# Kernel optimization log

Measured on AMD Instinct MI355X. Metric: run time of the kernel, lower is better.

Reference implementation:

```python
import jax, jax.numpy as jnp
import numpy as np

N = 20000      # nodes
E = 320000     # edges (before self-loops)
F_IN = 512     # input feature size
HID = 128      # encoder hidden
OUT = 128      # encoder output / GAT in_channels
H = 4          # gat heads
C = 64         # gat out_channels per head


def setup_inputs() -> dict:
    key = jax.random.key(0)
    ks = jax.random.split(key, 10)
    s = 0.05
    return {
        "x": jax.random.normal(ks[0], (N, F_IN), jnp.float32),
        "edge_index": jax.random.randint(ks[1], (2, E), 0, N, dtype=jnp.int64),
        "W1": jax.random.normal(ks[2], (F_IN, HID), jnp.float32) * s,
        "b1": jax.random.normal(ks[3], (HID,), jnp.float32) * s,
        "W2": jax.random.normal(ks[4], (HID, OUT), jnp.float32) * s,
        "b2": jax.random.normal(ks[5], (OUT,), jnp.float32) * s,
        "Wg": jax.random.normal(ks[6], (OUT, H * C), jnp.float32) * s,
        "att_src": jax.random.normal(ks[7], (H, C), jnp.float32) * s,
        "att_dst": jax.random.normal(ks[8], (H, C), jnp.float32) * s,
        "bias_g": jax.random.normal(ks[9], (H * C,), jnp.float32) * s,
    }


def reference(x, edge_index, W1, b1, W2, b2, Wg, att_src, att_dst, bias_g):
    # MLP encoder: Linear -> ReLU -> Linear
    h = jnp.maximum(x @ W1 + b1, 0.0) @ W2 + b2            # [N, OUT]

    # GATConv (concat=True, eval mode -> no dropout)
    xg = (h @ Wg).reshape(N, H, C)                          # per-head projections

    # add self-loops (PyG GATConv default)
    loops = jnp.arange(N, dtype=edge_index.dtype)
    src = jnp.concatenate([edge_index[0], loops])           # [E+N] source j
    dst = jnp.concatenate([edge_index[1], loops])           # [E+N] dest   i

    a_src = jnp.einsum('nhc,hc->nh', xg, att_src)           # [N, H]
    a_dst = jnp.einsum('nhc,hc->nh', xg, att_dst)           # [N, H]

    e = jax.nn.leaky_relu(a_src[src] + a_dst[dst], 0.2)     # [E+N, H]

    # segment softmax over incoming edges of each destination node
    m = jax.ops.segment_max(e, dst, num_segments=N)         # [N, H]
    ex = jnp.exp(e - m[dst])
    denom = jax.ops.segment_sum(ex, dst, num_segments=N)
    alpha = ex / (denom[dst] + 1e-16)                       # [E+N, H]

    # weighted scatter-add aggregation
    out = jax.ops.segment_sum(alpha[:, :, None] * xg[src], dst, num_segments=N)  # [N, H, C]
    return out.reshape(N, H * C) + bias_g
```

## Files before the change

### kernel.cpp

```cpp
#include <hip/hip_runtime.h>
#include <math.h>

#define NNODES 20000
#define NEDGES 320000
#define FIN    512
#define HIDD   128
#define OUTD   128
#define NH     4
#define NC     64
#define HC     256

typedef short bf16x8 __attribute__((ext_vector_type(8)));
typedef float f32x4  __attribute__((ext_vector_type(4)));

__device__ __forceinline__ unsigned short f2bf(float f) {
    unsigned int u = __float_as_uint(f);
    unsigned int r = 0x7fffu + ((u >> 16) & 1u);
    return (unsigned short)((u + r) >> 16);
}
__device__ __forceinline__ float b2f(short t) {
    return __uint_as_float(((unsigned)(unsigned short)t) << 16);
}

#define PREP_TB1 64
#define PREP_TB2 192
__global__ __launch_bounds__(256)
void prep_kernel(const float* __restrict__ W1, unsigned short* __restrict__ W1t,
                 const float* __restrict__ W2, const float* __restrict__ b2,
                 const float* __restrict__ Wg, unsigned short* __restrict__ W2gt,
                 float* __restrict__ b2g, int* __restrict__ deg, int n) {
    const int bid = blockIdx.x;
    const int tid = threadIdx.x;
    if (bid < PREP_TB1) {
        __shared__ float tile[32][33];
        const int tk = bid >> 2;
        const int tn = bid & 3;
        const int k0 = tk * 32, n0 = tn * 32;
        const int nin = tid & 31;
        const int r8  = tid >> 5;
        #pragma unroll
        for (int s = 0; s < 4; ++s) {
            int k = s * 8 + r8;
            tile[k][nin] = W1[(size_t)(k0 + k) * HIDD + n0 + nin];
        }
        __syncthreads();
        #pragma unroll
        for (int s = 0; s < 4; ++s) {
            int nn = s * 8 + r8;
            W1t[(size_t)(n0 + nn) * FIN + k0 + nin] = f2bf(tile[nin][nn]);
        }
    } else if (bid < PREP_TB2) {
        int local = (bid - PREP_TB1) * 256 + tid;
        int nn = local >> 7;
        int k  = local & 127;
        float s = 0.f;
        #pragma unroll 8
        for (int t = 0; t < HIDD; ++t)
            s += W2[(size_t)k * OUTD + t] * Wg[(size_t)t * HC + nn];
        W2gt[(size_t)nn * HIDD + k] = f2bf(s);
        if (k == 0) {
            float t2 = 0.f;
            #pragma unroll 8
            for (int t = 0; t < OUTD; ++t) t2 += b2[t] * Wg[(size_t)t * HC + nn];
            b2g[nn] = t2;
        }
    } else {
        int i = (bid - PREP_TB2) * 256 + tid;
        if (i < n) deg[i] = 1;
    }
}

__global__ __launch_bounds__(256)
void gemm1_count_kernel(const float* __restrict__ A,
                        const unsigned short* __restrict__ Bt,
                        const float* __restrict__ bias,
                        unsigned short* __restrict__ C,
                        const int* __restrict__ dst, int* __restrict__ deg,
                        int M, int E, int gemmBlocks) {
    __shared__ unsigned short As[32 * 64];
    __shared__ unsigned short Bs[128 * 64];

    if ((int)blockIdx.x >= gemmBlocks) {
        int base = ((int)blockIdx.x - gemmBlocks) * 1024 + threadIdx.x;
        #pragma unroll
        for (int t = 0; t < 4; ++t) {
            int i = base + t * 256;
            if (i < E) atomicAdd(&deg[dst[i]], 1);
        }
        return;
    }

    const int tid  = threadIdx.x;
    const int lane = tid & 63;
    const int w    = tid >> 6;
    const int wr   = w >> 1;
    const int wc   = w & 1;
    const int m0   = blockIdx.x * 32;

    char* pA = (char*)As;
    char* pB = (char*)Bs;

    f32x4 acc[4];
    #pragma unroll
    for (int n = 0; n < 4; ++n) acc[n] = (f32x4){0.f, 0.f, 0.f, 0.f};

    for (int k0 = 0; k0 < FIN; k0 += 64) {
        {
            const int row = tid >> 3;
            const int sg  = tid & 7;
            const bool ok = (m0 + row) < M;
            const float4* Ap = (const float4*)(A + (size_t)(m0 + row) * FIN + k0 + sg * 8);
            float4 f0 = make_float4(0,0,0,0), f1 = f0;
            if (ok) { f0 = Ap[0]; f1 = Ap[1]; }
            unsigned short u[8];
            u[0]=f2bf(f0.x); u[1]=f2bf(f0.y); u[2]=f2bf(f0.z); u[3]=f2bf(f0.w);
            u[4]=f2bf(f1.x); u[5]=f2bf(f1.y); u[6]=f2bf(f1.z); u[7]=f2bf(f1.w);
            *(bf16x8*)(pA + (((row * 128 + sg * 16)) ^ ((row & 7) << 4))) = *(bf16x8*)&u[0];
        }
        #pragma unroll
        for (int i = 0; i < 4; ++i) {
            int s   = tid + i * 256;
            int col = s >> 3;
            int sg  = s & 7;
            bf16x8 v = *(const bf16x8*)(Bt + (size_t)col * FIN + k0 + sg * 8);
            *(bf16x8*)(pB + (((col * 128 + sg * 16)) ^ ((col & 7) << 4))) = v;
        }
        __syncthreads();

        #pragma unroll
        for (int ks = 0; ks < 2; ++ks) {
            const int kb = ks * 64 + ((lane >> 4) << 4);
            int row = wr * 16 + (lane & 15);
            bf16x8 a = *(const bf16x8*)(pA + ((row * 128 + kb) ^ ((row & 7) << 4)));
            bf16x8 b[4];
            #pragma unroll
            for (int n = 0; n < 4; ++n) {
                int col = wc * 64 + n * 16 + (lane & 15);
                b[n] = *(const bf16x8*)(pB + ((col * 128 + kb) ^ ((col & 7) << 4)));
            }
            #pragma unroll
            for (int n = 0; n < 4; ++n)
                acc[n] = __builtin_amdgcn_mfma_f32_16x16x32_bf16(a, b[n], acc[n], 0, 0, 0);
        }
        __syncthreads();
    }

    #pragma unroll
    for (int n = 0; n < 4; ++n) {
        const int col = wc * 64 + n * 16 + (lane & 15);
        const float bv = bias[col];
        #pragma unroll
        for (int r = 0; r < 4; ++r) {
            const int row = m0 + wr * 16 + ((lane >> 4) << 2) + r;
            if (row >= M) continue;
            float v = fmaxf(acc[n][r] + bv, 0.f);
            C[(size_t)row * HIDD + col] = f2bf(v);
        }
    }
}

__global__ __launch_bounds__(1024)
void scan_offsets_kernel(const int* __restrict__ deg, int* __restrict__ offs,
                         int* __restrict__ cursor, int* __restrict__ csr, int n) {
    __shared__ int wsum[16], wbase[16];
    const int tid = threadIdx.x, lane = tid & 63, w = tid >> 6;
    const int i0 = tid * 20;
    int loc[20];
    int s = 0;
    #pragma unroll
    for (int k = 0; k < 20; ++k) {
        int i = i0 + k;
        int v = (i < n) ? deg[i] : 0;
        loc[k] = s;
        s += v;
    }
    int incl = s;
    #pragma unroll
    for (int d = 1; d < 64; d <<= 1) {
        int t = __shfl_up(incl, d);
        if (lane >= d) incl += t;
    }
    if (lane == 63) wsum[w] = incl;
    __syncthreads();
    if (w == 0) {
        int v = (lane < 16) ? wsum[lane] : 0;
        int sc = v;
        #pragma unroll
        for (int d = 1; d < 16; d <<= 1) {
            int t = __shfl_up(sc, d);
            if (lane >= d) sc += t;
        }
        if (lane < 16) wbase[lane] = sc - v;
    }
    __syncthreads();
    const int excl = wbase[w] + incl - s;
    #pragma unroll
    for (int k = 0; k < 20; ++k) {
        int i = i0 + k;
        if (i < n) {
            int o = excl + loc[k];
            offs[i]   = o;
            cursor[i] = o + 1;
            csr[o]    = i;
        }
    }
    if (tid == 1023) offs[n] = excl + s;
}

__global__ __launch_bounds__(256)
void gemm2_dots_scatter_kernel(const unsigned short* __restrict__ Ab,
                               const unsigned short* __restrict__ Bt,
                               const float* __restrict__ b2g,
                               const float* __restrict__ att_src,
                               const float* __restrict__ att_dst,
                               unsigned short* __restrict__ xgh,
                               float* __restrict__ a_src, float* __restrict__ a_dst,
                               const int* __restrict__ e_src, const int* __restrict__ e_dst,
                               int* __restrict__ cursor, int* __restrict__ csr,
                               int M, int E, int gemmBlocks) {
    const int tid = threadIdx.x;

    if ((int)blockIdx.x >= gemmBlocks) {
        int i = ((int)blockIdx.x - gemmBlocks) * 256 + tid;
        if (i < E) {
            int s = e_src[i], d = e_dst[i];
            csr[atomicAdd(&cursor[d], 1)] = s;
        }
        return;
    }

    __shared__ unsigned short As[64 * 64];
    __shared__ unsigned short Bs[128 * 64];

    const int lane = tid & 63;
    const int w    = tid >> 6;
    const int wr   = w >> 1;
    const int wc   = w & 1;
    const int m0   = ((int)blockIdx.x >> 1) * 64;
    const int n0   = ((int)blockIdx.x & 1) * 128;

    char* pA = (char*)As;
    char* pB = (char*)Bs;

    f32x4 acc[2][4];
    #pragma unroll
    for (int m = 0; m < 2; ++m)
        #pragma unroll
        for (int n = 0; n < 4; ++n) acc[m][n] = (f32x4){0.f, 0.f, 0.f, 0.f};

    for (int k0 = 0; k0 < HIDD; k0 += 64) {
        #pragma unroll
        for (int i = 0; i < 2; ++i) {
            int s   = tid + i * 256;
            int row = s >> 3;
            int sg  = s & 7;
            bf16x8 v = {};
            if ((m0 + row) < M)
                v = *(const bf16x8*)(Ab + (size_t)(m0 + row) * HIDD + k0 + sg * 8);
            *(bf16x8*)(pA + (((row * 128 + sg * 16)) ^ ((row & 7) << 4))) = v;
        }
        #pragma unroll
        for (int i = 0; i < 4; ++i) {
            int s   = tid + i * 256;
            int col = s >> 3;
            int sg  = s & 7;
            bf16x8 v = *(const bf16x8*)(Bt + (size_t)(n0 + col) * HIDD + k0 + sg * 8);
            *(bf16x8*)(pB + (((col * 128 + sg * 16)) ^ ((col & 7) << 4))) = v;
        }
        __syncthreads();

        #pragma unroll
        for (int ks = 0; ks < 2; ++ks) {
            const int kb = ks * 64 + ((lane >> 4) << 4);
            bf16x8 a[2], b[4];
            #pragma unroll
            for (int m = 0; m < 2; ++m) {
                int row = wr * 32 + m * 16 + (lane & 15);
                a[m] = *(const bf16x8*)(pA + ((row * 128 + kb) ^ ((row & 7) << 4)));
            }
            #pragma unroll
            for (int n = 0; n < 4; ++n) {
                int col = wc * 64 + n * 16 + (lane & 15);
                b[n] = *(const bf16x8*)(pB + ((col * 128 + kb) ^ ((col & 7) << 4)));
            }
            #pragma unroll
            for (int m = 0; m < 2; ++m)
                #pragma unroll
                for (int n = 0; n < 4; ++n)
                    acc[m][n] = __builtin_amdgcn_mfma_f32_16x16x32_bf16(
                        a[m], b[n], acc[m][n], 0, 0, 0);
        }
        __syncthreads();
    }

    const int head = ((int)blockIdx.x & 1) * 2 + wc;
    const int cIn  = lane & 15;
    unsigned short* plane = xgh + (size_t)head * M * NC;
    float ds_p[2][4], dd_p[2][4];
    #pragma unroll
    for (int m = 0; m < 2; ++m)
        #pragma unroll
        for (int r = 0; r < 4; ++r) { ds_p[m][r] = 0.f; dd_p[m][r] = 0.f; }

    #pragma unroll
    for (int n = 0; n < 4; ++n) {
        const int ch  = n * 16 + cIn;
        const int col = n0 + wc * 64 + n * 16 + cIn;
        const float bv   = b2g[col];
        const float as_c = att_src[head * NC + ch];
        const float ad_c = att_dst[head * NC + ch];
        #pragma unroll
        for (int m = 0; m < 2; ++m) {
            #pragma unroll
            for (int r = 0; r < 4; ++r) {
                const int row = m0 + wr * 32 + m * 16 + ((lane >> 4) << 2) + r;
                float v = acc[m][n][r] + bv;
                if (row < M) plane[(size_t)row * NC + ch] = f2bf(v);
                ds_p[m][r] += v * as_c;
                dd_p[m][r] += v * ad_c;
            }
        }
    }
    #pragma unroll
    for (int m = 0; m < 2; ++m) {
        #pragma unroll
        for (int r = 0; r < 4; ++r) {
            float s = ds_p[m][r], d = dd_p[m][r];
            s += __shfl_xor(s, 1); s += __shfl_xor(s, 2);
            s += __shfl_xor(s, 4); s += __shfl_xor(s, 8);
            d += __shfl_xor(d, 1); d += __shfl_xor(d, 2);
            d += __shfl_xor(d, 4); d += __shfl_xor(d, 8);
            if (cIn == 0) {
                const int row = m0 + wr * 32 + m * 16 + ((lane >> 4) << 2) + r;
                if (row < M) {
                    a_src[row * NH + head] = s;
                    a_dst[row * NH + head] = d;
                }
            }
        }
    }
}

__global__ __launch_bounds__(256)
void gat_aggregate6_kernel(const unsigned short* __restrict__ xgh,
                           const float* __restrict__ asrc,
                           const float* __restrict__ adst,
                           const int* __restrict__ offs, const int* __restrict__ csr,
                           const float* __restrict__ bias, float* __restrict__ out,
                           int n, int nbPerHead) {
    const int wv   = threadIdx.x >> 6;
    const int lane = threadIdx.x & 63;
    const int head = (int)blockIdx.x / nbPerHead;
    const int node = ((int)blockIdx.x % nbPerHead) * 4 + wv;
    if (node >= n) return;
    const int g = lane >> 3;
    const int q = lane & 7;
    const int beg = offs[node];
    const int deg = offs[node + 1] - beg;
    const float adh = adst[node * NH + head];
    const unsigned short* plane = xgh + (size_t)head * n * NC;

    float acc[8] = {0.f, 0.f, 0.f, 0.f, 0.f, 0.f, 0.f, 0.f};
    float den = 0.f;

    for (int c0 = 0; c0 < deg; c0 += 64) {
        const int j = c0 + lane;
        int   s_l = 0;
        float w_l = 0.f;
        if (j < deg) {
            s_l = csr[beg + j];
            float e = asrc[s_l * NH + head] + adh;
            e = e > 0.f ? e : 0.2f * e;
            w_l = __expf(e);
        }
        den += w_l;

        const int cn = (deg - c0 < 64) ? (deg - c0) : 64;
        #pragma unroll
        for (int t = 0; t < 8; ++t) {
            if (t * 8 >= cn) break;
            const int jj = t * 8 + g;
            const float wgt = __shfl(w_l, jj);
            const int   s   = __shfl(s_l, jj);
            if (jj < cn) {
                bf16x8 v = *(const bf16x8*)(plane + (size_t)s * NC + q * 8);
                #pragma unroll
                for (int u = 0; u < 8; ++u) acc[u] += wgt * b2f(v[u]);
            }
        }
    }

    #pragma unroll
    for (int mask = 1; mask <= 32; mask <<= 1) den += __shfl_xor(den, mask);
    #pragma unroll
    for (int mask = 8; mask <= 32; mask <<= 1) {
        #pragma unroll
        for (int t = 0; t < 8; ++t) acc[t] += __shfl_xor(acc[t], mask);
    }

    if (g == 0) {
        const float inv = 1.f / (den + 1e-16f);
        const int cb = head * NC + q * 8;
        const int base = node * HC + cb;
        float4 o0 = make_float4(acc[0] * inv + bias[cb + 0],
                                acc[1] * inv + bias[cb + 1],
                                acc[2] * inv + bias[cb + 2],
                                acc[3] * inv + bias[cb + 3]);
        float4 o1 = make_float4(acc[4] * inv + bias[cb + 4],
                                acc[5] * inv + bias[cb + 5],
                                acc[6] * inv + bias[cb + 6],
                                acc[7] * inv + bias[cb + 7]);
        *(float4*)(out + base)     = o0;
        *(float4*)(out + base + 4) = o1;
    }
}

extern "C" void kernel_launch(void* const* d_in, const int* in_sizes, int n_in,
                              void* d_out, int out_size, void* d_ws, size_t ws_size,
                              hipStream_t stream) {
    const float* x       = (const float*)d_in[0];
    const int*   ei      = (const int*)d_in[1];
    const float* W1      = (const float*)d_in[2];
    const float* b1      = (const float*)d_in[3];
    const float* W2      = (const float*)d_in[4];
    const float* b2      = (const float*)d_in[5];
    const float* Wg      = (const float*)d_in[6];
    const float* att_src = (const float*)d_in[7];
    const float* att_dst = (const float*)d_in[8];
    const float* bias_g  = (const float*)d_in[9];

    const int Nn = in_sizes[0] / FIN;
    const int E  = in_sizes[1] / 2;
    const int* e_src = ei;
    const int* e_dst = ei + E;

    char* w = (char*)d_ws;
    auto alloc = [&](size_t bytes) { char* p = w; w += (bytes + 255) & ~(size_t)255; return p; };
    unsigned short* W1t  = (unsigned short*)alloc((size_t)OUTD * FIN * 2);
    unsigned short* W2gt = (unsigned short*)alloc((size_t)HC * HIDD * 2);
    float* b2g  = (float*)alloc(HC * 4);
    unsigned short* h1  = (unsigned short*)alloc((size_t)Nn * HIDD * 2);
    unsigned short* xgh = (unsigned short*)alloc((size_t)NH * Nn * NC * 2);
    float* asrc = (float*)alloc((size_t)Nn * NH * 4);
    float* adst = (float*)alloc((size_t)Nn * NH * 4);
    int* deg    = (int*)alloc((size_t)Nn * 4);
    int* offs   = (int*)alloc((size_t)(Nn + 1) * 4);
    int* cursor = (int*)alloc((size_t)Nn * 4);
    int* csr    = (int*)alloc((size_t)(E + Nn) * 4);

    dim3 blk(256);

    {
        int nb = PREP_TB2 + (Nn + 255) / 256;
        prep_kernel<<<dim3(nb), blk, 0, stream>>>(
            W1, W1t, W2, b2, Wg, W2gt, b2g, deg, Nn);
    }

    {
        int gb = (Nn + 31) / 32;
        int cb = (E + 1023) / 1024;
        gemm1_count_kernel<<<dim3(gb + cb), blk, 0, stream>>>(
            x, W1t, b1, h1, e_dst, deg, Nn, E, gb);
    }

    scan_offsets_kernel<<<dim3(1), dim3(1024), 0, stream>>>(deg, offs, cursor, csr, Nn);

    {
        int gb = ((Nn + 63) / 64) * 2;
        int sb = (E + 255) / 256;
        gemm2_dots_scatter_kernel<<<dim3(gb + sb), blk, 0, stream>>>(
            h1, W2gt, b2g, att_src, att_dst, xgh, asrc, adst,
            e_src, e_dst, cursor, csr, Nn, E, gb);
    }

    {
        int nbPerHead = (Nn + 3) / 4;
        gat_aggregate6_kernel<<<dim3(NH * nbPerHead), blk, 0, stream>>>(
            xgh, asrc, adst, offs, csr, bias_g, (float*)d_out, Nn, nbPerHead);
    }
}
```

Before: 137.4 us.

## Use 16-bit CSR indices, head-major attention scores, move degree counting to prep

Stores CSR source indices as 16-bit values, which relies on the node count fitting in 16 bits. Switches a_src/a_dst to a head-major layout so each aggregate wave gathers from a contiguous per-head array. Degree counting moves from the gemm1 launch into the prep kernel, with a memset replacing the init-to-one and the +1 for self-loops added in the scan. Bf16 unpacking also switches to uint4 lo/hi bit tricks. The aim is to cut gather bandwidth in aggregation, at the cost of an extra memset launch and an index width that limits the node count.

Measured after the change: 141.8 us. +3.3%, slower.

```diff
diff --git a/kernel.cpp b/kernel.cpp
--- a/kernel.cpp
+++ b/kernel.cpp
@@ -18,17 +18,21 @@
     unsigned int r = 0x7fffu + ((u >> 16) & 1u);
     return (unsigned short)((u + r) >> 16);
 }
-__device__ __forceinline__ float b2f(short t) {
-    return __uint_as_float(((unsigned)(unsigned short)t) << 16);
+__device__ __forceinline__ float bflo(unsigned int u) {
+    return __uint_as_float(u << 16);
+}
+__device__ __forceinline__ float bfhi(unsigned int u) {
+    return __uint_as_float(u & 0xffff0000u);
 }
 
 #define PREP_TB1 64
 #define PREP_TB2 192
 __global__ __launch_bounds__(256)
-void prep_kernel(const float* __restrict__ W1, unsigned short* __restrict__ W1t,
-                 const float* __restrict__ W2, const float* __restrict__ b2,
-                 const float* __restrict__ Wg, unsigned short* __restrict__ W2gt,
-                 float* __restrict__ b2g, int* __restrict__ deg, int n) {
+void prep_count_kernel(const float* __restrict__ W1, unsigned short* __restrict__ W1t,
+                       const float* __restrict__ W2, const float* __restrict__ b2,
+                       const float* __restrict__ Wg, unsigned short* __restrict__ W2gt,
+                       float* __restrict__ b2g,
+                       const int* __restrict__ e_dst, int* __restrict__ deg, int E) {
     const int bid = blockIdx.x;
     const int tid = threadIdx.x;
     if (bid < PREP_TB1) {
@@ -66,29 +70,17 @@
         }
     } else {
         int i = (bid - PREP_TB2) * 256 + tid;
-        if (i < n) deg[i] = 1;
+        if (i < E) atomicAdd(&deg[e_dst[i]], 1);
     }
 }
 
 __global__ __launch_bounds__(256)
-void gemm1_count_kernel(const float* __restrict__ A,
-                        const unsigned short* __restrict__ Bt,
-                        const float* __restrict__ bias,
-                        unsigned short* __restrict__ C,
-                        const int* __restrict__ dst, int* __restrict__ deg,
-                        int M, int E, int gemmBlocks) {
+void gemm1_kernel(const float* __restrict__ A,
+                  const unsigned short* __restrict__ Bt,
+                  const float* __restrict__ bias,
+                  unsigned short* __restrict__ C, int M) {
     __shared__ unsigned short As[32 * 64];
     __shared__ unsigned short Bs[128 * 64];
-
-    if ((int)blockIdx.x >= gemmBlocks) {
-        int base = ((int)blockIdx.x - gemmBlocks) * 1024 + threadIdx.x;
-        #pragma unroll
-        for (int t = 0; t < 4; ++t) {
-            int i = base + t * 256;
-            if (i < E) atomicAdd(&deg[dst[i]], 1);
-        }
-        return;
-    }
 
     const int tid  = threadIdx.x;
     const int lane = tid & 63;
@@ -161,7 +153,8 @@
 
 __global__ __launch_bounds__(1024)
 void scan_offsets_kernel(const int* __restrict__ deg, int* __restrict__ offs,
-                         int* __restrict__ cursor, int* __restrict__ csr, int n) {
+                         int* __restrict__ cursor, unsigned short* __restrict__ csr16,
+                         int n) {
     __shared__ int wsum[16], wbase[16];
     const int tid = threadIdx.x, lane = tid & 63, w = tid >> 6;
     const int i0 = tid * 20;
@@ -170,7 +163,7 @@
     #pragma unroll
     for (int k = 0; k < 20; ++k) {
         int i = i0 + k;
-        int v = (i < n) ? deg[i] : 0;
+        int v = (i < n) ? (deg[i] + 1) : 0;
         loc[k] = s;
         s += v;
     }
@@ -199,9 +192,9 @@
         int i = i0 + k;
         if (i < n) {
             int o = excl + loc[k];
-            offs[i]   = o;
-            cursor[i] = o + 1;
-            csr[o]    = i;
+            offs[i]    = o;
+            cursor[i]  = o + 1;
+            csr16[o]   = (unsigned short)i;
         }
     }
     if (tid == 1023) offs[n] = excl + s;
@@ -214,9 +207,10 @@
                                const float* __restrict__ att_src,
                                const float* __restrict__ att_dst,
                                unsigned short* __restrict__ xgh,
-                               float* __restrict__ a_src, float* __restrict__ a_dst,
+                               float* __restrict__ a_src,
+                               float* __restrict__ a_dst,
                                const int* __restrict__ e_src, const int* __restrict__ e_dst,
-                               int* __restrict__ cursor, int* __restrict__ csr,
+                               int* __restrict__ cursor, unsigned short* __restrict__ csr16,
                                int M, int E, int gemmBlocks) {
     const int tid = threadIdx.x;
 
@@ -224,7 +218,7 @@
         int i = ((int)blockIdx.x - gemmBlocks) * 256 + tid;
         if (i < E) {
             int s = e_src[i], d = e_dst[i];
-            csr[atomicAdd(&cursor[d], 1)] = s;
+            csr16[atomicAdd(&cursor[d], 1)] = (unsigned short)s;
         }
         return;
     }
@@ -333,8 +327,8 @@
             if (cIn == 0) {
                 const int row = m0 + wr * 32 + m * 16 + ((lane >> 4) << 2) + r;
                 if (row < M) {
-                    a_src[row * NH + head] = s;
-                    a_dst[row * NH + head] = d;
+                    a_src[(size_t)head * M + row] = s;
+                    a_dst[(size_t)head * M + row] = d;
                 }
             }
         }
@@ -342,10 +336,11 @@
 }
 
 __global__ __launch_bounds__(256)
-void gat_aggregate6_kernel(const unsigned short* __restrict__ xgh,
-                           const float* __restrict__ asrc,
-                           const float* __restrict__ adst,
-                           const int* __restrict__ offs, const int* __restrict__ csr,
+void gat_aggregate7_kernel(const unsigned short* __restrict__ xgh,
+                           const float* __restrict__ asrc_h,
+                           const float* __restrict__ adst_h,
+                           const int* __restrict__ offs,
+                           const unsigned short* __restrict__ csr16,
                            const float* __restrict__ bias, float* __restrict__ out,
                            int n, int nbPerHead) {
     const int wv   = threadIdx.x >> 6;
@@ -357,7 +352,8 @@
     const int q = lane & 7;
     const int beg = offs[node];
     const int deg = offs[node + 1] - beg;
-    const float adh = adst[node * NH + head];
+    const float* asp = asrc_h + (size_t)head * n;
+    const float adh = adst_h[(size_t)head * n + node];
     const unsigned short* plane = xgh + (size_t)head * n * NC;
 
     float acc[8] = {0.f, 0.f, 0.f, 0.f, 0.f, 0.f, 0.f, 0.f};
@@ -368,8 +364,8 @@
         int   s_l = 0;
         float w_l = 0.f;
         if (j < deg) {
-            s_l = csr[beg + j];
-            float e = asrc[s_l * NH + head] + adh;
+            s_l = csr16[beg + j];
+            float e = asp[s_l] + adh;
             e = e > 0.f ? e : 0.2f * e;
             w_l = __expf(e);
         }
@@ -383,9 +379,11 @@
             const float wgt = __shfl(w_l, jj);
             const int   s   = __shfl(s_l, jj);
             if (jj < cn) {
-                bf16x8 v = *(const bf16x8*)(plane + (size_t)s * NC + q * 8);
-                #pragma unroll
-                for (int u = 0; u < 8; ++u) acc[u] += wgt * b2f(v[u]);
+                const uint4 u = *(const uint4*)(plane + ((size_t)s << 6) + q * 8);
+                acc[0] += wgt * bflo(u.x); acc[1] += wgt * bfhi(u.x);
+                acc[2] += wgt * bflo(u.y); acc[3] += wgt * bfhi(u.y);
+                acc[4] += wgt * bflo(u.z); acc[5] += wgt * bfhi(u.z);
+                acc[6] += wgt * bflo(u.w); acc[7] += wgt * bfhi(u.w);
             }
         }
     }
@@ -441,41 +439,38 @@
     float* b2g  = (float*)alloc(HC * 4);
     unsigned short* h1  = (unsigned short*)alloc((size_t)Nn * HIDD * 2);
     unsigned short* xgh = (unsigned short*)alloc((size_t)NH * Nn * NC * 2);
-    float* asrc = (float*)alloc((size_t)Nn * NH * 4);
-    float* adst = (float*)alloc((size_t)Nn * NH * 4);
+    float* asrc = (float*)alloc((size_t)NH * Nn * 4);
+    float* adst = (float*)alloc((size_t)NH * Nn * 4);
     int* deg    = (int*)alloc((size_t)Nn * 4);
     int* offs   = (int*)alloc((size_t)(Nn + 1) * 4);
     int* cursor = (int*)alloc((size_t)Nn * 4);
-    int* csr    = (int*)alloc((size_t)(E + Nn) * 4);
+    unsigned short* csr16 = (unsigned short*)alloc((size_t)(E + Nn) * 2);
 
     dim3 blk(256);
 
+    hipMemsetAsync(deg, 0, (size_t)Nn * 4, stream);
+
     {
-        int nb = PREP_TB2 + (Nn + 255) / 256;
-        prep_kernel<<<dim3(nb), blk, 0, stream>>>(
-            W1, W1t, W2, b2, Wg, W2gt, b2g, deg, Nn);
-    }
-
-    {
-        int gb = (Nn + 31) / 32;
-        int cb = (E + 1023) / 1024;
-        gemm1_count_kernel<<<dim3(gb + cb), blk, 0, stream>>>(
-            x, W1t, b1, h1, e_dst, deg, Nn, E, gb);
-    }
-
-    scan_offsets_kernel<<<dim3(1), dim3(1024), 0, stream>>>(deg, offs, cursor, csr, Nn);
+        int nb = PREP_TB2 + (E + 255) / 256;
+        prep_count_kernel<<<dim3(nb), blk, 0, stream>>>(
+            W1, W1t, W2, b2, Wg, W2gt, b2g, e_dst, deg, E);
+    }
+
+    gemm1_kernel<<<dim3((Nn + 31) / 32), blk, 0, stream>>>(x, W1t, b1, h1, Nn);
+
+    scan_offsets_kernel<<<dim3(1), dim3(1024), 0, stream>>>(deg, offs, cursor, csr16, Nn);
 
     {
         int gb = ((Nn + 63) / 64) * 2;
         int sb = (E + 255) / 256;
         gemm2_dots_scatter_kernel<<<dim3(gb + sb), blk, 0, stream>>>(
             h1, W2gt, b2g, att_src, att_dst, xgh, asrc, adst,
-            e_src, e_dst, cursor, csr, Nn, E, gb);
+            e_src, e_dst, cursor, csr16, Nn, E, gb);
     }
 
     {
         int nbPerHead = (Nn + 3) / 4;
-        gat_aggregate6_kernel<<<dim3(NH * nbPerHead), blk, 0, stream>>>(
-            xgh, asrc, adst, offs, csr, bias_g, (float*)d_out, Nn, nbPerHead);
-    }
-}
+        gat_aggregate7_kernel<<<dim3(NH * nbPerHead), blk, 0, stream>>>(
+            xgh, asrc, adst, offs, csr16, bias_g, (float*)d_out, Nn, nbPerHead);
+    }
+}
```
